# Performance work log

Measured on AMD Instinct MI355X. Metric: run time of the kernel, lower is better.

Reference implementation:

```python
import jax, jax.numpy as jnp
import numpy as np
from jax import lax

NPOINT, RADIUS, NSAMPLE, K_KEY = 64, 1.0, 32, 64

def conv1d(x, W, b):
    # 1x1 Conv1d: x [B,Cin,N], W [Cout,Cin], b [Cout] -> [B,Cout,N]
    return jnp.einsum('bcn,dc->bdn', x, W) + b[None, :, None]

def farthest_point_sample(xyz, npoint):
    # xyz [B,N,3] -> idx [B,npoint]
    B, N, _ = xyz.shape
    dist0 = jnp.full((B, N), 1e10, dtype=xyz.dtype)
    far0 = jnp.zeros((B,), dtype=jnp.int32)
    def body(carry, _):
        dist, far = carry
        centroid = jnp.take_along_axis(xyz, far[:, None, None].astype(jnp.int32), axis=1)  # [B,1,3]
        d = jnp.sum((xyz - centroid) ** 2, -1)
        dist = jnp.minimum(dist, d)
        nxt = jnp.argmax(dist, -1).astype(jnp.int32)
        return (dist, nxt), far
    _, idxs = lax.scan(body, (dist0, far0), None, length=npoint)
    return idxs.T  # [B,npoint]

def ball_query(radius, nsample, xyz, new_xyz):
    # xyz [B,N,3], new_xyz [B,S,3] -> group_idx [B,S,nsample]
    N = xyz.shape[1]
    sqr = jnp.sum((new_xyz[:, :, None, :] - xyz[:, None, :, :]) ** 2, -1)  # [B,S,N]
    gidx = jnp.where(sqr > radius ** 2, N, jnp.arange(N, dtype=jnp.int32)[None, None, :])
    gidx = jnp.sort(gidx, axis=-1)[..., :nsample]
    first = gidx[..., :1]
    gidx = jnp.where(gidx == N, first, gidx)
    return gidx

def sample_and_group(npoint, radius, nsample, xyz, points):
    # xyz [B,N,3], points [B,N,D]
    B = xyz.shape[0]
    fps_idx = farthest_point_sample(xyz, npoint)                     # [B,S]
    bidx = jnp.arange(B)[:, None]
    new_xyz = xyz[bidx, fps_idx]                                     # [B,S,3]
    gidx = ball_query(radius, nsample, xyz, new_xyz)                 # [B,S,ns]
    bidx2 = jnp.arange(B)[:, None, None]
    grouped_xyz = xyz[bidx2, gidx]                                   # [B,S,ns,3]
    grouped_xyz_norm = grouped_xyz - new_xyz[:, :, None, :]
    grouped_points = points[bidx2, gidx]                             # [B,S,ns,D]
    new_points = jnp.concatenate([grouped_xyz_norm, grouped_points], axis=-1)
    return new_xyz, new_points

def setup_inputs() -> dict:
    key = jax.random.key(0)
    ks = jax.random.split(key, 12)
    B, C, N = 8, 6, 65536
    def w(k, co, ci):
        return jax.random.normal(k, (co, ci), jnp.float32) * (1.0 / np.sqrt(ci))
    return {
        'src_pts': jax.random.normal(ks[0], (B, C, N), jnp.float32),
        'tgt_pts': jax.random.normal(ks[1], (B, C, N), jnp.float32),
        'W1': w(ks[2], 32, 6),  'b1': jnp.zeros((32,), jnp.float32),
        'W2': w(ks[3], 64, 32), 'b2': jnp.zeros((64,), jnp.float32),
        'Wa': w(ks[4], 16, 64), 'ba': jnp.zeros((16,), jnp.float32),
        'Wb': w(ks[5], 8, 16),  'bb': jnp.zeros((8,), jnp.float32),
        'Wc': w(ks[6], 1, 8),   'bc': jnp.zeros((1,), jnp.float32),
    }

def reference(src_pts, tgt_pts, W1, b1, W2, b2, Wa, ba, Wb, bb, Wc, bc):
    # feat_extraction_layer: 1x1 conv stack over points -> deep per-point features
    h = jax.nn.relu(conv1d(src_pts, W1, b1))            # [B,32,N]
    deep_feat_pts = jax.nn.relu(conv1d(h, W2, b2))      # [B,64,N]
    # weighting_layer: per-point saliency weight + top-k keypoint indices (1-D, batch-0 idiom)
    w = jax.nn.relu(conv1d(deep_feat_pts, Wa, ba))
    w = jax.nn.relu(conv1d(w, Wb, bb))
    w = jax.nn.softplus(conv1d(w, Wc, bc))              # [B,1,N]
    _, keypts_idx = lax.top_k(w[0, 0], K_KEY)           # [K]
    # irregular keypoint gather (shared index across batch, as in src_pts[:, :, idx])
    src_keypts = src_pts[:, :, keypts_idx].transpose(0, 2, 1)   # [B,K,C]
    # ball-query sample_and_group on keypoints (computed then discarded, as in original)
    _gxyz, _gpts = sample_and_group(NPOINT, RADIUS, NSAMPLE, src_keypts[:, :, :3], src_keypts[:, :, 3:])
    return src_keypts
```

## Files before the change

### kernel.cpp

```cpp
#include <hip/hip_runtime.h>
#include <stdint.h>

#define N_PTS 65536
#define NB1 32768
#define NB2 4096
#define CAND_CAP 4096
#define FCAP 1024
typedef unsigned long long u64;


__global__ __launch_bounds__(256) void zero_kernel(uint4* __restrict__ z, int n4)
{
    const int i = blockIdx.x * 256 + threadIdx.x;
    const uint4 zz = {0u, 0u, 0u, 0u};
    if (i < n4) z[i] = zz;
}

__global__ __launch_bounds__(512, 1) void score_kernel(
    const float* __restrict__ src,
    const float* __restrict__ W1, const float* __restrict__ b1,
    const float* __restrict__ W2, const float* __restrict__ b2,
    const float* __restrict__ Wa, const float* __restrict__ ba,
    const float* __restrict__ Wb, const float* __restrict__ bb,
    const float* __restrict__ Wc, const float* __restrict__ bc,
    float* __restrict__ scores, unsigned* __restrict__ hist1)
{
    __shared__ unsigned histL[NB1];
    __shared__ __align__(16) float sW1[32 * 8];
    __shared__ __align__(16) float sW2[64 * 32];
    __shared__ __align__(16) float sWaT[64 * 16];
    __shared__ __align__(16) float sWb[8 * 16];
    __shared__ float sb2[64], sba[16], sbb[8], sWc[8], sbc1[1];
    const int t = threadIdx.x;

    {
        uint4* h4 = (uint4*)histL;
        const uint4 zz = {0u, 0u, 0u, 0u};
        #pragma unroll
        for (int i = 0; i < 16; i++) h4[t + 512 * i] = zz;
    }
    if (t < 256) {
        const int j = t >> 3, c = t & 7;
        sW1[t] = (c < 6) ? W1[j * 6 + c] : ((c == 6) ? b1[j] : 0.f);
    }
    for (int i = t; i < 2048; i += 512) sW2[i] = W2[i];
    for (int i = t; i < 1024; i += 512) {
        const int j = i >> 4, q = i & 15;
        sWaT[i] = Wa[q * 64 + j];
    }
    if (t < 128) sWb[t] = Wb[t];
    if (t < 64)  sb2[t] = b2[t];
    if (t < 16)  sba[t] = ba[t];
    if (t < 8)   { sbb[t] = bb[t]; sWc[t] = Wc[t]; }
    if (t == 0)  sbc1[0] = bc[0];
    __syncthreads();

    const int base = blockIdx.x * 1024;
    const int p[2] = { base + t, base + 512 + t };

    float x[2][6];
    #pragma unroll
    for (int c = 0; c < 6; c++) {
        x[0][c] = src[c * N_PTS + p[0]];
        x[1][c] = src[c * N_PTS + p[1]];
    }

    float h1[2][32];
    #pragma unroll
    for (int j = 0; j < 32; j++) {
        const float4 wA = *(const float4*)&sW1[j * 8];
        const float4 wB = *(const float4*)&sW1[j * 8 + 4];
        #pragma unroll
        for (int P = 0; P < 2; P++) {
            float a = wB.z;
            a = fmaf(wA.x, x[P][0], a); a = fmaf(wA.y, x[P][1], a);
            a = fmaf(wA.z, x[P][2], a); a = fmaf(wA.w, x[P][3], a);
            a = fmaf(wB.x, x[P][4], a); a = fmaf(wB.y, x[P][5], a);
            h1[P][j] = fmaxf(a, 0.f);
        }
    }

    float h3[2][16];
    #pragma unroll
    for (int q = 0; q < 16; q++) { h3[0][q] = sba[q]; h3[1][q] = sba[q]; }

    #pragma unroll 1
    for (int jb = 0; jb < 32; jb++) {
        const int j0 = 2 * jb, j1 = j0 + 1;
        const float4* r0 = (const float4*)&sW2[j0 * 32];
        const float4* r1 = (const float4*)&sW2[j1 * 32];
        const float4* wa0 = (const float4*)&sWaT[j0 * 16];
        const float4* wa1 = (const float4*)&sWaT[j1 * 16];
        float4 u[8], v[8], q0[4], q1[4];
        #pragma unroll
        for (int i = 0; i < 8; i++) u[i] = r0[i];
        #pragma unroll
        for (int i = 0; i < 8; i++) v[i] = r1[i];
        #pragma unroll
        for (int i = 0; i < 4; i++) q0[i] = wa0[i];
        #pragma unroll
        for (int i = 0; i < 4; i++) q1[i] = wa1[i];
        const float bj0 = sb2[j0], bj1 = sb2[j1];

        #pragma unroll
        for (int P = 0; P < 2; P++) {
            float a0 = 0.f, a1 = 0.f, a2 = 0.f, a3 = 0.f;
            float c0 = 0.f, c1 = 0.f, c2 = 0.f, c3 = 0.f;
            #pragma unroll
            for (int i4 = 0; i4 < 8; i4++) {
                const float h0 = h1[P][4 * i4 + 0], hh1 = h1[P][4 * i4 + 1];
                const float h2 = h1[P][4 * i4 + 2], hh3 = h1[P][4 * i4 + 3];
                a0 = fmaf(u[i4].x, h0, a0); a1 = fmaf(u[i4].y, hh1, a1);
                a2 = fmaf(u[i4].z, h2, a2); a3 = fmaf(u[i4].w, hh3, a3);
                c0 = fmaf(v[i4].x, h0, c0); c1 = fmaf(v[i4].y, hh1, c1);
                c2 = fmaf(v[i4].z, h2, c2); c3 = fmaf(v[i4].w, hh3, c3);
            }
            const float v0 = fmaxf((a0 + a1) + (a2 + a3) + bj0, 0.f);
            const float v1 = fmaxf((c0 + c1) + (c2 + c3) + bj1, 0.f);
            #pragma unroll
            for (int q4 = 0; q4 < 4; q4++) {
                float t0 = h3[P][4 * q4 + 0], t1 = h3[P][4 * q4 + 1];
                float t2 = h3[P][4 * q4 + 2], t3 = h3[P][4 * q4 + 3];
                t0 = fmaf(q0[q4].x, v0, t0); t1 = fmaf(q0[q4].y, v0, t1);
                t2 = fmaf(q0[q4].z, v0, t2); t3 = fmaf(q0[q4].w, v0, t3);
                t0 = fmaf(q1[q4].x, v1, t0); t1 = fmaf(q1[q4].y, v1, t1);
                t2 = fmaf(q1[q4].z, v1, t2); t3 = fmaf(q1[q4].w, v1, t3);
                h3[P][4 * q4 + 0] = t0; h3[P][4 * q4 + 1] = t1;
                h3[P][4 * q4 + 2] = t2; h3[P][4 * q4 + 3] = t3;
            }
        }
    }
    #pragma unroll
    for (int q = 0; q < 16; q++) {
        h3[0][q] = fmaxf(h3[0][q], 0.f);
        h3[1][q] = fmaxf(h3[1][q], 0.f);
    }

    float z[2] = { sbc1[0], sbc1[0] };
    #pragma unroll
    for (int j = 0; j < 8; j++) {
        const float4* wbr = (const float4*)&sWb[j * 16];
        const float4 w0 = wbr[0], w1 = wbr[1], w2 = wbr[2], w3 = wbr[3];
        const float bj = sbb[j], wc = sWc[j];
        #pragma unroll
        for (int P = 0; P < 2; P++) {
            float s0 = bj, s1 = 0.f, s2 = 0.f, s3 = 0.f;
            s0 = fmaf(w0.x, h3[P][0],  s0); s1 = fmaf(w0.y, h3[P][1],  s1);
            s2 = fmaf(w0.z, h3[P][2],  s2); s3 = fmaf(w0.w, h3[P][3],  s3);
            s0 = fmaf(w1.x, h3[P][4],  s0); s1 = fmaf(w1.y, h3[P][5],  s1);
            s2 = fmaf(w1.z, h3[P][6],  s2); s3 = fmaf(w1.w, h3[P][7],  s3);
            s0 = fmaf(w2.x, h3[P][8],  s0); s1 = fmaf(w2.y, h3[P][9],  s1);
            s2 = fmaf(w2.z, h3[P][10], s2); s3 = fmaf(w2.w, h3[P][11], s3);
            s0 = fmaf(w3.x, h3[P][12], s0); s1 = fmaf(w3.y, h3[P][13], s1);
            s2 = fmaf(w3.z, h3[P][14], s2); s3 = fmaf(w3.w, h3[P][15], s3);
            z[P] = fmaf(wc, fmaxf((s0 + s1) + (s2 + s3), 0.f), z[P]);
        }
    }

    #pragma unroll
    for (int P = 0; P < 2; P++) {
        const float sp = fmaxf(z[P], 0.f) + log1pf(expf(-fabsf(z[P])));
        scores[p[P]] = sp;
        atomicAdd(&histL[__float_as_uint(sp) >> 16], 1u);
    }
    __syncthreads();

    {
        const uint4* h4 = (const uint4*)histL;
        for (int i = t; i < NB1 / 4; i += 512) {
            const uint4 v = h4[i];
            if (v.x) atomicAdd(&hist1[4 * i + 0], v.x);
            if (v.y) atomicAdd(&hist1[4 * i + 1], v.y);
            if (v.z) atomicAdd(&hist1[4 * i + 2], v.z);
            if (v.w) atomicAdd(&hist1[4 * i + 3], v.w);
        }
    }
}

__global__ __launch_bounds__(256) void refine_kernel(
    const unsigned* __restrict__ hist1, const float* __restrict__ scores,
    unsigned* __restrict__ hist2, int* __restrict__ meta,
    u64* __restrict__ cand, const float* __restrict__ src,
    float* __restrict__ out)
{
    __shared__ unsigned csum[256];
    __shared__ unsigned bsum[128];
    __shared__ unsigned h2[NB2];
    __shared__ u64 keys[FCAP];
    __shared__ int idxs[64];
    __shared__ int sh_c, sh_B, sh_T2, sh_cnt;
    __shared__ unsigned sh_tail, sh_rank;
    const int t = threadIdx.x;

    {
        unsigned s = 0;
        const uint4* h4 = (const uint4*)(hist1 + t * 128);
        #pragma unroll
        for (int i = 0; i < 32; i++) {
            const uint4 v = h4[i];
            s += v.x + v.y + v.z + v.w;
        }
        csum[t] = s;
    }
    __syncthreads();
    for (int d = 1; d < 256; d <<= 1) {
        const unsigned v = (t + d < 256) ? csum[t + d] : 0u;
        __syncthreads();
        csum[t] += v;
        __syncthreads();
    }
    {
        const unsigned here = csum[t];
        const unsigned nxt = (t + 1 < 256) ? csum[t + 1] : 0u;
        if (here >= 64u && nxt < 64u) sh_c = t;
    }
    __syncthreads();
    const int cstar = sh_c;
    if (t < 128) bsum[t] = hist1[cstar * 128 + t];
    __syncthreads();
    {
        const unsigned ctail = (cstar + 1 < 256) ? csum[cstar + 1] : 0u;
        for (int d = 1; d < 128; d <<= 1) {
            unsigned v = 0u;
            if (t < 128 && t + d < 128) v = bsum[t + d];
            __syncthreads();
            if (t < 128) bsum[t] += v;
            __syncthreads();
        }
        if (t < 128) {
            const unsigned here = bsum[t] + ctail;
            const unsigned nxt = (t + 1 < 128) ? bsum[t + 1] + ctail : ctail;
            if (here >= 64u && nxt < 64u) { sh_B = cstar * 128 + t; sh_tail = nxt; }
        }
    }
    __syncthreads();
    const unsigned Bstar = (unsigned)sh_B;
    const unsigned tail1 = sh_tail;

    {
        const float4* s4 = (const float4*)scores;
        const int i = blockIdx.x * 256 + t;
        const float4 v = s4[i];
        const int n0 = 4 * i;
        #pragma unroll
        for (int k = 0; k < 4; k++) {
            const float sv = (k == 0) ? v.x : (k == 1) ? v.y : (k == 2) ? v.z : v.w;
            const unsigned b = __float_as_uint(sv);
            const unsigned hi = b >> 16;
            if (hi >= Bstar) {
                const int p = atomicAdd(&meta[2], 1);
                if (p < CAND_CAP) cand[p] = ((u64)b << 32) | (unsigned)~(n0 + k);
                if (hi == Bstar) atomicAdd(&hist2[(b & 0xFFFFu) >> 4], 1u);
            }
        }
    }

    __syncthreads();
    __threadfence();
    if (t == 0) sh_rank = atomicAdd((unsigned*)&meta[3], 1u);
    __syncthreads();
    if (sh_rank != 63u) return;
    __threadfence();

    {
        uint4* d = (uint4*)h2;
        const uint4* s = (const uint4*)hist2;
        #pragma unroll
        for (int i = 0; i < 4; i++) d[t + 256 * i] = s[t + 256 * i];
    }
    __syncthreads();

    {
        unsigned s = 0;
        #pragma unroll
        for (int i = 0; i < 16; i++) s += h2[t * 16 + i];
        csum[t] = s;
    }
    __syncthreads();
    for (int d = 1; d < 256; d <<= 1) {
        const unsigned v = (t + d < 256) ? csum[t + d] : 0u;
        __syncthreads();
        csum[t] += v;
        __syncthreads();
    }
    {
        const unsigned here = tail1 + csum[t];
        const unsigned nxt = tail1 + ((t + 1 < 256) ? csum[t + 1] : 0u);
        if (here >= 64u && nxt < 64u) sh_c = t;
    }
    __syncthreads();
    {
        const int c2 = sh_c;
        if (t == 0) {
            unsigned acc = tail1 + ((c2 + 1 < 256) ? csum[c2 + 1] : 0u);
            int T2 = c2 * 16;
            for (int b = c2 * 16 + 15; b >= c2 * 16; b--) {
                acc += h2[b];
                if (acc >= 64u) { T2 = b; break; }
            }
            sh_T2 = T2;
            sh_cnt = 0;
        }
    }
    __syncthreads();
    const unsigned T2 = (unsigned)sh_T2;

    int count = meta[2];
    if (count > CAND_CAP) count = CAND_CAP;
    for (int i = t; i < count; i += 256) {
        const u64 key = cand[i];
        const unsigned b = (unsigned)(key >> 32);
        const unsigned hi = b >> 16;
        if (hi > Bstar || ((b & 0xFFFFu) >> 4) >= T2) {
            const int p = atomicAdd(&sh_cnt, 1);
            if (p < FCAP) keys[p] = key;
        }
    }
    __syncthreads();

    int fcnt = sh_cnt;
    if (fcnt > FCAP) fcnt = FCAP;
    for (int i = t; i < fcnt; i += 256) {
        const u64 me = keys[i];
        int r = 0;
        for (int j = 0; j < fcnt; j++) r += (keys[j] > me);
        if (r < 64) idxs[r] = (int)~(unsigned)(me & 0xFFFFFFFFu);
    }
    __syncthreads();

    for (int e = t; e < 3072; e += 256) {
        const int b  = e / 384;
        const int rr = e % 384;
        const int kk = rr / 6;
        const int c  = rr % 6;
        out[e] = src[(b * 6 + c) * N_PTS + idxs[kk]];
    }
}

extern "C" void kernel_launch(void* const* d_in, const int* in_sizes, int n_in,
                              void* d_out, int out_size, void* d_ws, size_t ws_size,
                              hipStream_t stream)
{
    const float* src = (const float*)d_in[0];
    const float* W1 = (const float*)d_in[2];
    const float* b1 = (const float*)d_in[3];
    const float* W2 = (const float*)d_in[4];
    const float* b2 = (const float*)d_in[5];
    const float* Wa = (const float*)d_in[6];
    const float* ba = (const float*)d_in[7];
    const float* Wb = (const float*)d_in[8];
    const float* bb = (const float*)d_in[9];
    const float* Wc = (const float*)d_in[10];
    const float* bc = (const float*)d_in[11];

    char* ws = (char*)d_ws;
    float*    scores = (float*)ws;
    unsigned* hist1  = (unsigned*)(ws + 256 * 1024);
    unsigned* hist2  = (unsigned*)(ws + 384 * 1024);
    int*      meta   = (int*)(ws + 400 * 1024);
    u64*      cand   = (u64*)(ws + 408 * 1024);
    float*    out    = (float*)d_out;

    const int n4 = (NB1 + NB2 + 16) / 4;
    zero_kernel<<<(n4 + 255) / 256, 256, 0, stream>>>((uint4*)hist1, n4);
    score_kernel<<<64, 512, 0, stream>>>(src, W1, b1, W2, b2, Wa, ba,
                                         Wb, bb, Wc, bc, scores, hist1);
    refine_kernel<<<64, 256, 0, stream>>>(hist1, scores, hist2, meta, cand,
                                          src, out);
}
```

Before: 144.0 us.

## Rebalance score kernel to 128 blocks of 128 threads with 4 points each

The score kernel goes from 64 blocks of 512 threads handling 2 points per thread to 128 blocks of 128 threads handling 4 points per thread. The fused conv2/conva loop now processes one output channel at a time across 4 points, which raises weight reuse per LDS read. More blocks spread the work over more CUs. In exchange, each block zeroes and flushes a full 32K-bin shared histogram with fewer threads, and there are twice as many global histogram merges.

Measured after the change: 164.1 us. 1.14x slower.

```diff
diff --git a/kernel.cpp b/kernel.cpp
--- a/kernel.cpp
+++ b/kernel.cpp
@@ -16,7 +16,7 @@
     if (i < n4) z[i] = zz;
 }
 
-__global__ __launch_bounds__(512, 1) void score_kernel(
+__global__ __launch_bounds__(128, 1) void score_kernel(
     const float* __restrict__ src,
     const float* __restrict__ W1, const float* __restrict__ b1,
     const float* __restrict__ W2, const float* __restrict__ b2,
@@ -37,14 +37,14 @@
         uint4* h4 = (uint4*)histL;
         const uint4 zz = {0u, 0u, 0u, 0u};
         #pragma unroll
-        for (int i = 0; i < 16; i++) h4[t + 512 * i] = zz;
-    }
-    if (t < 256) {
-        const int j = t >> 3, c = t & 7;
-        sW1[t] = (c < 6) ? W1[j * 6 + c] : ((c == 6) ? b1[j] : 0.f);
-    }
-    for (int i = t; i < 2048; i += 512) sW2[i] = W2[i];
-    for (int i = t; i < 1024; i += 512) {
+        for (int i = 0; i < 64; i++) h4[t + 128 * i] = zz;
+    }
+    for (int i = t; i < 256; i += 128) {
+        const int j = i >> 3, c = i & 7;
+        sW1[i] = (c < 6) ? W1[j * 6 + c] : ((c == 6) ? b1[j] : 0.f);
+    }
+    for (int i = t; i < 2048; i += 128) sW2[i] = W2[i];
+    for (int i = t; i < 1024; i += 128) {
         const int j = i >> 4, q = i & 15;
         sWaT[i] = Wa[q * 64 + j];
     }
@@ -55,23 +55,25 @@
     if (t == 0)  sbc1[0] = bc[0];
     __syncthreads();
 
-    const int base = blockIdx.x * 1024;
-    const int p[2] = { base + t, base + 512 + t };
-
-    float x[2][6];
+    const int base = blockIdx.x * 512;
+    int p[4];
+    #pragma unroll
+    for (int P = 0; P < 4; P++) p[P] = base + 128 * P + t;
+
+    float x[4][6];
     #pragma unroll
     for (int c = 0; c < 6; c++) {
-        x[0][c] = src[c * N_PTS + p[0]];
-        x[1][c] = src[c * N_PTS + p[1]];
-    }
-
-    float h1[2][32];
-    #pragma unroll
+        #pragma unroll
+        for (int P = 0; P < 4; P++) x[P][c] = src[c * N_PTS + p[P]];
+    }
+
+    float h1[4][32];
+    #pragma unroll 8
     for (int j = 0; j < 32; j++) {
         const float4 wA = *(const float4*)&sW1[j * 8];
         const float4 wB = *(const float4*)&sW1[j * 8 + 4];
         #pragma unroll
-        for (int P = 0; P < 2; P++) {
+        for (int P = 0; P < 4; P++) {
             float a = wB.z;
             a = fmaf(wA.x, x[P][0], a); a = fmaf(wA.y, x[P][1], a);
             a = fmaf(wA.z, x[P][2], a); a = fmaf(wA.w, x[P][3], a);
@@ -80,70 +82,63 @@
         }
     }
 
-    float h3[2][16];
-    #pragma unroll
-    for (int q = 0; q < 16; q++) { h3[0][q] = sba[q]; h3[1][q] = sba[q]; }
-
-    #pragma unroll 1
-    for (int jb = 0; jb < 32; jb++) {
-        const int j0 = 2 * jb, j1 = j0 + 1;
-        const float4* r0 = (const float4*)&sW2[j0 * 32];
-        const float4* r1 = (const float4*)&sW2[j1 * 32];
-        const float4* wa0 = (const float4*)&sWaT[j0 * 16];
-        const float4* wa1 = (const float4*)&sWaT[j1 * 16];
-        float4 u[8], v[8], q0[4], q1[4];
-        #pragma unroll
-        for (int i = 0; i < 8; i++) u[i] = r0[i];
-        #pragma unroll
-        for (int i = 0; i < 8; i++) v[i] = r1[i];
-        #pragma unroll
-        for (int i = 0; i < 4; i++) q0[i] = wa0[i];
-        #pragma unroll
-        for (int i = 0; i < 4; i++) q1[i] = wa1[i];
-        const float bj0 = sb2[j0], bj1 = sb2[j1];
-
-        #pragma unroll
-        for (int P = 0; P < 2; P++) {
+    float h3[4][16];
+    #pragma unroll
+    for (int q = 0; q < 16; q++) {
+        const float b = sba[q];
+        h3[0][q] = b; h3[1][q] = b; h3[2][q] = b; h3[3][q] = b;
+    }
+
+    #pragma unroll 2
+    for (int j = 0; j < 64; j++) {
+        const float4* w2r = (const float4*)&sW2[j * 32];
+        const float4* war = (const float4*)&sWaT[j * 16];
+        float4 w[8], wq[4];
+        #pragma unroll
+        for (int i = 0; i < 8; i++) w[i] = w2r[i];
+        #pragma unroll
+        for (int i = 0; i < 4; i++) wq[i] = war[i];
+        const float bj = sb2[j];
+
+        float v[4];
+        #pragma unroll
+        for (int P = 0; P < 4; P++) {
             float a0 = 0.f, a1 = 0.f, a2 = 0.f, a3 = 0.f;
-            float c0 = 0.f, c1 = 0.f, c2 = 0.f, c3 = 0.f;
             #pragma unroll
             for (int i4 = 0; i4 < 8; i4++) {
-                const float h0 = h1[P][4 * i4 + 0], hh1 = h1[P][4 * i4 + 1];
-                const float h2 = h1[P][4 * i4 + 2], hh3 = h1[P][4 * i4 + 3];
-                a0 = fmaf(u[i4].x, h0, a0); a1 = fmaf(u[i4].y, hh1, a1);
-                a2 = fmaf(u[i4].z, h2, a2); a3 = fmaf(u[i4].w, hh3, a3);
-                c0 = fmaf(v[i4].x, h0, c0); c1 = fmaf(v[i4].y, hh1, c1);
-                c2 = fmaf(v[i4].z, h2, c2); c3 = fmaf(v[i4].w, hh3, c3);
+                a0 = fmaf(w[i4].x, h1[P][4 * i4 + 0], a0);
+                a1 = fmaf(w[i4].y, h1[P][4 * i4 + 1], a1);
+                a2 = fmaf(w[i4].z, h1[P][4 * i4 + 2], a2);
+                a3 = fmaf(w[i4].w, h1[P][4 * i4 + 3], a3);
             }
-            const float v0 = fmaxf((a0 + a1) + (a2 + a3) + bj0, 0.f);
-            const float v1 = fmaxf((c0 + c1) + (c2 + c3) + bj1, 0.f);
+            v[P] = fmaxf((a0 + a1) + (a2 + a3) + bj, 0.f);
+        }
+        #pragma unroll
+        for (int q4 = 0; q4 < 4; q4++) {
+            const float4 ww = wq[q4];
             #pragma unroll
-            for (int q4 = 0; q4 < 4; q4++) {
-                float t0 = h3[P][4 * q4 + 0], t1 = h3[P][4 * q4 + 1];
-                float t2 = h3[P][4 * q4 + 2], t3 = h3[P][4 * q4 + 3];
-                t0 = fmaf(q0[q4].x, v0, t0); t1 = fmaf(q0[q4].y, v0, t1);
-                t2 = fmaf(q0[q4].z, v0, t2); t3 = fmaf(q0[q4].w, v0, t3);
-                t0 = fmaf(q1[q4].x, v1, t0); t1 = fmaf(q1[q4].y, v1, t1);
-                t2 = fmaf(q1[q4].z, v1, t2); t3 = fmaf(q1[q4].w, v1, t3);
-                h3[P][4 * q4 + 0] = t0; h3[P][4 * q4 + 1] = t1;
-                h3[P][4 * q4 + 2] = t2; h3[P][4 * q4 + 3] = t3;
+            for (int P = 0; P < 4; P++) {
+                h3[P][4 * q4 + 0] = fmaf(ww.x, v[P], h3[P][4 * q4 + 0]);
+                h3[P][4 * q4 + 1] = fmaf(ww.y, v[P], h3[P][4 * q4 + 1]);
+                h3[P][4 * q4 + 2] = fmaf(ww.z, v[P], h3[P][4 * q4 + 2]);
+                h3[P][4 * q4 + 3] = fmaf(ww.w, v[P], h3[P][4 * q4 + 3]);
             }
         }
     }
     #pragma unroll
     for (int q = 0; q < 16; q++) {
-        h3[0][q] = fmaxf(h3[0][q], 0.f);
-        h3[1][q] = fmaxf(h3[1][q], 0.f);
-    }
-
-    float z[2] = { sbc1[0], sbc1[0] };
+        #pragma unroll
+        for (int P = 0; P < 4; P++) h3[P][q] = fmaxf(h3[P][q], 0.f);
+    }
+
+    float z[4] = { sbc1[0], sbc1[0], sbc1[0], sbc1[0] };
     #pragma unroll
     for (int j = 0; j < 8; j++) {
         const float4* wbr = (const float4*)&sWb[j * 16];
         const float4 w0 = wbr[0], w1 = wbr[1], w2 = wbr[2], w3 = wbr[3];
         const float bj = sbb[j], wc = sWc[j];
         #pragma unroll
-        for (int P = 0; P < 2; P++) {
+        for (int P = 0; P < 4; P++) {
             float s0 = bj, s1 = 0.f, s2 = 0.f, s3 = 0.f;
             s0 = fmaf(w0.x, h3[P][0],  s0); s1 = fmaf(w0.y, h3[P][1],  s1);
             s2 = fmaf(w0.z, h3[P][2],  s2); s3 = fmaf(w0.w, h3[P][3],  s3);
@@ -158,7 +153,7 @@
     }
 
     #pragma unroll
-    for (int P = 0; P < 2; P++) {
+    for (int P = 0; P < 4; P++) {
         const float sp = fmaxf(z[P], 0.f) + log1pf(expf(-fabsf(z[P])));
         scores[p[P]] = sp;
         atomicAdd(&histL[__float_as_uint(sp) >> 16], 1u);
@@ -167,7 +162,7 @@
 
     {
         const uint4* h4 = (const uint4*)histL;
-        for (int i = t; i < NB1 / 4; i += 512) {
+        for (int i = t; i < NB1 / 4; i += 128) {
             const uint4 v = h4[i];
             if (v.x) atomicAdd(&hist1[4 * i + 0], v.x);
             if (v.y) atomicAdd(&hist1[4 * i + 1], v.y);
@@ -363,8 +358,8 @@
 
     const int n4 = (NB1 + NB2 + 16) / 4;
     zero_kernel<<<(n4 + 255) / 256, 256, 0, stream>>>((uint4*)hist1, n4);
-    score_kernel<<<64, 512, 0, stream>>>(src, W1, b1, W2, b2, Wa, ba,
-                                         Wb, bb, Wc, bc, scores, hist1);
+    score_kernel<<<128, 128, 0, stream>>>(src, W1, b1, W2, b2, Wa, ba,
+                                          Wb, bb, Wc, bc, scores, hist1);
     refine_kernel<<<64, 256, 0, stream>>>(hist1, scores, hist2, meta, cand,
                                           src, out);
 }
```
